# Kernel optimization log

Hardware: AMD Instinct MI355X
Metric: run time of the kernel (lower is better)

## Reference

```python
import jax, jax.numpy as jnp
import numpy as np

WS = 8      # window_size
SS = 4      # shift_size
DIM = 64
B, H, W = 4, 256, 256
EPS = 1e-12


def _conv(x, w, groups=1, pad=0):
    return jax.lax.conv_general_dilated(
        x, w, window_strides=(1, 1), padding=[(pad, pad), (pad, pad)],
        feature_group_count=groups,
        dimension_numbers=('NCHW', 'OIHW', 'NCHW'))


def _window_partition(x, ws):
    # Faithful to torch: permute (B,C,nh,ws,nw,ws)->(B,C,nh,nw,ws,ws) then flat view(-1,C,ws,ws)
    b, c, h, w = x.shape
    pb, pr = (-h) % ws, (-w) % ws
    if pb or pr:
        x = jnp.pad(x, ((0, 0), (0, 0), (0, pb), (0, pr)))
    h2, w2 = h + pb, w + pr
    x = x.reshape(b, c, h2 // ws, ws, w2 // ws, ws).transpose(0, 1, 2, 4, 3, 5)
    return x.reshape(-1, c, ws, ws)


def _window_reverse(win, ws, h, w):
    pb, pr = (-h) % ws, (-w) % ws
    h2, w2 = h + pb, w + pr
    b = win.shape[0] * ws * ws // (h2 * w2)
    x = win.reshape(b, -1, h2 // ws, w2 // ws, ws, ws).transpose(0, 1, 2, 4, 3, 5)
    x = x.reshape(b, -1, h2, w2)
    return x[:, :, :h, :w]


def _chan_attn(q, k, v, temp):
    # channel (transposed) attention on flattened window pixels
    n, c = q.shape[0], q.shape[1]
    q = q.reshape(n, c, -1)
    k = k.reshape(n, c, -1)
    v = v.reshape(n, c, -1)
    q = q / jnp.maximum(jnp.linalg.norm(q, axis=-1, keepdims=True), EPS)
    k = k / jnp.maximum(jnp.linalg.norm(k, axis=-1, keepdims=True), EPS)
    attn = jax.nn.softmax(jnp.einsum('ncd,nkd->nck', q, k) / temp, axis=-1)
    out = jnp.einsum('nck,nkd->ncd', attn, v)
    return out.reshape(n, c, WS, WS)


def setup_inputs() -> dict:
    key = jax.random.key(0)
    ks = jax.random.split(key, 10)
    C = DIM
    p = lambda k, s: jax.random.normal(k, s, jnp.float32) * 0.05
    return {
        'x': jax.random.normal(ks[0], (B, C, H, W), jnp.float32),
        'x_f': jax.random.normal(ks[1], (B, C, H, W), jnp.float32),
        'temperature': jnp.ones((1,), jnp.float32),
        'qk_w': p(ks[2], (2 * C, C, 1, 1)),
        'qk_dw_w': p(ks[3], (2 * C, 1, 3, 3)),
        'v_w': p(ks[4], (C, C, 1, 1)),
        'v_dw_w': p(ks[5], (C, 1, 3, 3)),
        'proj_w': p(ks[6], (C, C, 3, 3)),
        'proj1_w': p(ks[7], (C, C, 3, 3)),
        'qkv1_w': p(ks[8], (3 * C, C, 1, 1)),
        'qkv1_dw_w': p(ks[9], (3 * C, 1, 3, 3)),
    }


def reference(x, x_f, temperature, qk_w, qk_dw_w, v_w, v_dw_w,
              proj_w, proj1_w, qkv1_w, qkv1_dw_w):
    b, c, h, w = x.shape
    xw = _window_partition(x, WS)
    xfw = _window_partition(x_f, WS)

    qk = _conv(_conv(xfw, qk_w), qk_dw_w, groups=2 * c, pad=1)
    v = _conv(_conv(xw, v_w), v_dw_w, groups=c, pad=1)
    q, k = jnp.split(qk, 2, axis=1)
    out = _chan_attn(q, k, v, temperature)
    out = _conv(out, proj_w, pad=1)
    out = _window_reverse(out, WS, h, w)

    shift = jnp.roll(out, (-SS, -SS), axis=(2, 3))
    sw = _window_partition(shift, WS)
    qkv = _conv(_conv(sw, qkv1_w), qkv1_dw_w, groups=3 * c, pad=1)
    q, k, v = jnp.split(qkv, 3, axis=1)
    out = _chan_attn(q, k, v, temperature)
    out = _conv(out, proj1_w, pad=1)
    out = _window_reverse(out, WS, h, w)
    out = jnp.roll(out, (SS, SS), axis=(2, 3))
    return out
```

## Files before the change

### kernel.cpp

```cpp
#include <hip/hip_runtime.h>
#include <hip/hip_fp16.h>

typedef short v8s __attribute__((ext_vector_type(8)));
typedef float v4f __attribute__((ext_vector_type(4)));

#define MFMA_B16(a, b, c) __builtin_amdgcn_mfma_f32_16x16x32_bf16((a), (b), (c), 0, 0, 0)

#define XS 72
#define TS 68

__device__ __forceinline__ unsigned short bfr(float x) {
    unsigned u = __float_as_uint(x);
    u += 0x7fffu + ((u >> 16) & 1u);
    return (unsigned short)(u >> 16);
}

__device__ __forceinline__ void mm_stage_g(const unsigned short* __restrict__ Ag,
                                           const unsigned short* __restrict__ XB,
                                           float* __restrict__ T,
                                           int wv, int L, int q)
{
    v4f C[4];
#pragma unroll
    for (int nt = 0; nt < 4; ++nt) C[nt] = (v4f){0.f, 0.f, 0.f, 0.f};
#pragma unroll
    for (int kt = 0; kt < 2; ++kt) {
        v8s a = *(const v8s*)(Ag + (16 * wv + L) * 64 + kt * 32 + q * 8);
#pragma unroll
        for (int nt = 0; nt < 4; ++nt) {
            v8s b = *(const v8s*)(XB + (nt * 16 + L) * XS + kt * 32 + q * 8);
            C[nt] = MFMA_B16(a, b, C[nt]);
        }
    }
    const int rowb = 16 * wv + q * 4;
#pragma unroll
    for (int r = 0; r < 4; ++r) {
#pragma unroll
        for (int nt = 0; nt < 4; ++nt)
            T[(rowb + r) * TS + nt * 16 + L] = C[nt][r];
    }
}

template <bool TR, bool NORM>
__device__ __forceinline__ void dw_stage(const float* __restrict__ T,
                                         const float* __restrict__ dwg,
                                         unsigned short* __restrict__ M,
                                         int wv, int lane)
{
    const int c  = 16 * wv + (lane >> 2);
    const int r0 = (lane & 3) << 1;
    float w[9];
#pragma unroll
    for (int k = 0; k < 9; ++k) w[k] = dwg[c * 9 + k];
    float in[4][10];
#pragma unroll
    for (int r = 0; r < 4; ++r) {
        const int rr = r0 - 1 + r;
        in[r][0] = 0.f; in[r][9] = 0.f;
        if ((unsigned)rr < 8u) {
            float4 a = *(const float4*)(T + c * TS + rr * 8);
            float4 b = *(const float4*)(T + c * TS + rr * 8 + 4);
            in[r][1] = a.x; in[r][2] = a.y; in[r][3] = a.z; in[r][4] = a.w;
            in[r][5] = b.x; in[r][6] = b.y; in[r][7] = b.z; in[r][8] = b.w;
        } else {
#pragma unroll
            for (int j = 1; j < 9; ++j) in[r][j] = 0.f;
        }
    }
    float o[2][8];
#pragma unroll
    for (int rr = 0; rr < 2; ++rr)
#pragma unroll
        for (int j = 0; j < 8; ++j) {
            float s;
            s = w[0] * in[rr][j];
            s = fmaf(w[1], in[rr][j + 1], s);
            s = fmaf(w[2], in[rr][j + 2], s);
            s = fmaf(w[3], in[rr + 1][j], s);
            s = fmaf(w[4], in[rr + 1][j + 1], s);
            s = fmaf(w[5], in[rr + 1][j + 2], s);
            s = fmaf(w[6], in[rr + 2][j], s);
            s = fmaf(w[7], in[rr + 2][j + 1], s);
            s = fmaf(w[8], in[rr + 2][j + 2], s);
            o[rr][j] = s;
        }
    if (NORM) {
        float ss = 0.f;
#pragma unroll
        for (int rr = 0; rr < 2; ++rr)
#pragma unroll
            for (int j = 0; j < 8; ++j) ss = fmaf(o[rr][j], o[rr][j], ss);
        ss += __shfl_xor(ss, 1);
        ss += __shfl_xor(ss, 2);
        const float sc = 1.0f / fmaxf(sqrtf(ss), 1e-12f);
#pragma unroll
        for (int rr = 0; rr < 2; ++rr)
#pragma unroll
            for (int j = 0; j < 8; ++j) o[rr][j] *= sc;
    }
    if (TR) {
#pragma unroll
        for (int rr = 0; rr < 2; ++rr)
#pragma unroll
            for (int j = 0; j < 8; ++j)
                M[((r0 + rr) * 8 + j) * XS + c] = bfr(o[rr][j]);
    } else {
#pragma unroll
        for (int rr = 0; rr < 2; ++rr) {
            v8s v;
#pragma unroll
            for (int j = 0; j < 8; ++j) v[j] = (short)bfr(o[rr][j]);
            *(v8s*)(M + c * XS + (r0 + rr) * 8) = v;
        }
    }
}

__device__ __forceinline__ void mm_lds(const unsigned short* __restrict__ Am,
                                       const unsigned short* __restrict__ Bm,
                                       int wv, int L, int q, v4f C[4])
{
#pragma unroll
    for (int nt = 0; nt < 4; ++nt) C[nt] = (v4f){0.f, 0.f, 0.f, 0.f};
#pragma unroll
    for (int kt = 0; kt < 2; ++kt) {
        v8s a = *(const v8s*)(Am + (16 * wv + L) * XS + kt * 32 + q * 8);
#pragma unroll
        for (int nt = 0; nt < 4; ++nt) {
            v8s b = *(const v8s*)(Bm + (nt * 16 + L) * XS + kt * 32 + q * 8);
            C[nt] = MFMA_B16(a, b, C[nt]);
        }
    }
}

__device__ __forceinline__ void proj_mm(const unsigned short* __restrict__ Wg,
                                        const unsigned short* __restrict__ Ot,
                                        int wv, int L, int q, v4f C[4])
{
#pragma unroll
    for (int nt = 0; nt < 4; ++nt) C[nt] = (v4f){0.f, 0.f, 0.f, 0.f};
    const unsigned short* arow = Wg + (16 * wv + L) * 576;
    const int pc  = L & 7;
    const int prb = L >> 3;
#pragma unroll
    for (int tap = 0; tap < 9; ++tap) {
        const int dy = tap / 3 - 1, dx = tap % 3 - 1;
        const int spc = pc + dx;
        const bool vc = (unsigned)spc < 8u;
#pragma unroll
        for (int half = 0; half < 2; ++half) {
            v8s a = *(const v8s*)(arow + tap * 64 + half * 32 + q * 8);
#pragma unroll
            for (int nt = 0; nt < 4; ++nt) {
                const int spr = nt * 2 + prb + dy;
                v8s b = {0, 0, 0, 0, 0, 0, 0, 0};
                if (vc && (unsigned)spr < 8u)
                    b = *(const v8s*)(Ot + (spr * 8 + spc) * XS + half * 32 + q * 8);
                C[nt] = MFMA_B16(a, b, C[nt]);
            }
        }
    }
}

__device__ __forceinline__ void softmax_to_lds(v4f S[4], float invt,
                                               unsigned short* __restrict__ Am,
                                               int rowb, int L)
{
#pragma unroll
    for (int nt = 0; nt < 4; ++nt) S[nt] *= invt;
#pragma unroll
    for (int r = 0; r < 4; ++r) {
        float mx = fmaxf(fmaxf(S[0][r], S[1][r]), fmaxf(S[2][r], S[3][r]));
        mx = fmaxf(mx, __shfl_xor(mx, 1));
        mx = fmaxf(mx, __shfl_xor(mx, 2));
        mx = fmaxf(mx, __shfl_xor(mx, 4));
        mx = fmaxf(mx, __shfl_xor(mx, 8));
        float e0 = __expf(S[0][r] - mx);
        float e1 = __expf(S[1][r] - mx);
        float e2 = __expf(S[2][r] - mx);
        float e3 = __expf(S[3][r] - mx);
        float sm = e0 + e1 + e2 + e3;
        sm += __shfl_xor(sm, 1);
        sm += __shfl_xor(sm, 2);
        sm += __shfl_xor(sm, 4);
        sm += __shfl_xor(sm, 8);
        const float ri = 1.0f / sm;
        Am[(rowb + r) * XS + L +  0] = bfr(e0 * ri);
        Am[(rowb + r) * XS + L + 16] = bfr(e1 * ri);
        Am[(rowb + r) * XS + L + 32] = bfr(e2 * ri);
        Am[(rowb + r) * XS + L + 48] = bfr(e3 * ri);
    }
}

__global__ void prep(const float* __restrict__ qk_w, const float* __restrict__ v_w,
                     const float* __restrict__ qkv_w, const float* __restrict__ pw0,
                     const float* __restrict__ pw1, unsigned short* __restrict__ Wb)
{
    int i = blockIdx.x * 256 + threadIdx.x;
    float v;
    if (i < 8192) v = qk_w[i];
    else if (i < 12288) v = v_w[i - 8192];
    else if (i < 24576) v = qkv_w[i - 12288];
    else {
        int j = i - 24576;
        const float* s = pw0;
        if (j >= 36864) { s = pw1; j -= 36864; }
        const int o = j / 576, kk = j % 576;
        const int tap = kk >> 6, c = kk & 63;
        v = s[o * 576 + c * 9 + tap];
    }
    Wb[i] = bfr(v);
}

__global__ __launch_bounds__(256, 3) void k1(
    const float* __restrict__ x, const float* __restrict__ xf,
    const float* __restrict__ temp_p,
    const float* __restrict__ qk_dw, const float* __restrict__ v_dw,
    const unsigned short* __restrict__ Wqk, const unsigned short* __restrict__ Wv,
    const unsigned short* __restrict__ Wp0,
    __half* __restrict__ midh)
{
    __shared__ unsigned short XB[64 * XS];
    __shared__ float T[64 * TS];
    __shared__ unsigned short M0[64 * XS], M1[64 * XS], M2[64 * XS];

    const int t = threadIdx.x, n = blockIdx.x;
    const int lane = t & 63, wv = t >> 6, L = lane & 15, q = lane >> 4;
    const int rowb = 16 * wv + q * 4;
    const size_t base = (size_t)n << 12;
    const float invt = 1.0f / temp_p[0];

    const int yp = t >> 4, xx0 = (t & 15) << 4;
    const int c2b = (yp >> 3) << 5, ir = (yp & 7) << 3;

    {
        const float* src = xf + base + yp * 256 + xx0;
#pragma unroll
        for (int k = 0; k < 4; ++k) {
            float4 a = *(const float4*)(src + 4 * k);
            const int xx = xx0 + 4 * k;
            const int c = c2b + (xx >> 3), pb = ir + (xx & 7);
            XB[(pb + 0) * XS + c] = bfr(a.x);
            XB[(pb + 1) * XS + c] = bfr(a.y);
            XB[(pb + 2) * XS + c] = bfr(a.z);
            XB[(pb + 3) * XS + c] = bfr(a.w);
        }
    }
    __syncthreads();
    mm_stage_g(Wqk, XB, T, wv, L, q);
    __syncthreads();
    dw_stage<false, true>(T, qk_dw, M0, wv, lane);
    __syncthreads();
    mm_stage_g(Wqk + 4096, XB, T, wv, L, q);
    __syncthreads();
    dw_stage<false, true>(T, qk_dw + 576, M1, wv, lane);
    __syncthreads();

    float4 rx[4];
    {
        const float* src = x + base + yp * 256 + xx0;
#pragma unroll
        for (int k = 0; k < 4; ++k) rx[k] = *(const float4*)(src + 4 * k);
    }
    v4f S[4];
    mm_lds(M0, M1, wv, L, q, S);
    softmax_to_lds(S, invt, M0, rowb, L);
    {
#pragma unroll
        for (int k = 0; k < 4; ++k) {
            const int xx = xx0 + 4 * k;
            const int c = c2b + (xx >> 3), pb = ir + (xx & 7);
            XB[(pb + 0) * XS + c] = bfr(rx[k].x);
            XB[(pb + 1) * XS + c] = bfr(rx[k].y);
            XB[(pb + 2) * XS + c] = bfr(rx[k].z);
            XB[(pb + 3) * XS + c] = bfr(rx[k].w);
        }
    }
    __syncthreads();
    mm_stage_g(Wv, XB, T, wv, L, q);
    __syncthreads();
    dw_stage<true, false>(T, v_dw, M2, wv, lane);
    __syncthreads();
    v4f O[4];
    mm_lds(M0, M2, wv, L, q, O);
#pragma unroll
    for (int nt = 0; nt < 4; ++nt)
#pragma unroll
        for (int r = 0; r < 4; ++r)
            M1[(L + 16 * nt) * XS + (rowb + r)] = bfr(O[nt][r]);
    __syncthreads();
    v4f C[4];
    proj_mm(Wp0, M1, wv, L, q, C);
#pragma unroll
    for (int nt = 0; nt < 4; ++nt)
#pragma unroll
        for (int r = 0; r < 4; ++r) {
            const int o = rowb + r, p = L + 16 * nt;
            const int yy = ((o >> 5) << 3) + (p >> 3);
            const int xp = ((o & 31) << 3) + (p & 7);
            midh[base + yy * 256 + xp] = __float2half(C[nt][r]);
        }
}

__global__ __launch_bounds__(256, 3) void k2(
    const __half* __restrict__ midh, const float* __restrict__ temp_p,
    const float* __restrict__ qkv_dw,
    const unsigned short* __restrict__ Wqkv, const unsigned short* __restrict__ Wp1,
    float* __restrict__ out)
{
    __shared__ unsigned short XB[64 * XS];
    __shared__ float T[64 * TS];
    __shared__ unsigned short M0[64 * XS], M1[64 * XS], M2[64 * XS];

    const int t = threadIdx.x, m = blockIdx.x;
    const int lane = t & 63, wv = t >> 6, L = lane & 15, q = lane >> 4;
    const int rowb = 16 * wv + q * 4;
    const int plane = m >> 4, mh2 = m & 15;
    const __half* img = midh + ((size_t)plane << 16);
    const float invt = 1.0f / temp_p[0];

    {
        const int yp = t >> 4, xx0 = (t & 15) << 4;
        const int row = (mh2 * 16 + 4 + yp) & 255;
        const int c2b = (yp >> 3) << 5, ir = (yp & 7) << 3;
#pragma unroll
        for (int k = 0; k < 4; ++k) {
            const int cc = (xx0 + 4 + 4 * k) & 255;
            const __half2* hp = (const __half2*)(img + row * 256 + cc);
            __half2 h0 = hp[0], h1 = hp[1];
            const int xx = xx0 + 4 * k;
            const int c = c2b + (xx >> 3), pb = ir + (xx & 7);
            XB[(pb + 0) * XS + c] = bfr(__half2float(h0.x));
            XB[(pb + 1) * XS + c] = bfr(__half2float(h0.y));
            XB[(pb + 2) * XS + c] = bfr(__half2float(h1.x));
            XB[(pb + 3) * XS + c] = bfr(__half2float(h1.y));
        }
    }
    __syncthreads();
    mm_stage_g(Wqkv, XB, T, wv, L, q);
    __syncthreads();
    dw_stage<false, true>(T, qkv_dw, M0, wv, lane);
    __syncthreads();
    mm_stage_g(Wqkv + 4096, XB, T, wv, L, q);
    __syncthreads();
    dw_stage<false, true>(T, qkv_dw + 576, M1, wv, lane);
    __syncthreads();
    mm_stage_g(Wqkv + 8192, XB, T, wv, L, q);
    __syncthreads();
    dw_stage<true, false>(T, qkv_dw + 1152, M2, wv, lane);
    __syncthreads();
    v4f S[4];
    mm_lds(M0, M1, wv, L, q, S);
    softmax_to_lds(S, invt, M0, rowb, L);
    __syncthreads();
    v4f O[4];
    mm_lds(M0, M2, wv, L, q, O);
#pragma unroll
    for (int nt = 0; nt < 4; ++nt)
#pragma unroll
        for (int r = 0; r < 4; ++r)
            M1[(L + 16 * nt) * XS + (rowb + r)] = bfr(O[nt][r]);
    __syncthreads();
    v4f C[4];
    proj_mm(Wp1, M1, wv, L, q, C);
    float* op = out + ((size_t)plane << 16);
#pragma unroll
    for (int nt = 0; nt < 4; ++nt)
#pragma unroll
        for (int r = 0; r < 4; ++r) {
            const int o = rowb + r, p = L + 16 * nt;
            const int R = mh2 * 16 + ((o >> 5) << 3) + (p >> 3);
            const int orow = (R + 4) & 255;
            const int ocol = ((o & 31) * 8 + (p & 7) + 4) & 255;
            op[orow * 256 + ocol] = C[nt][r];
        }
}

extern "C" void kernel_launch(void* const* d_in, const int* in_sizes, int n_in,
                              void* d_out, int out_size, void* d_ws, size_t ws_size,
                              hipStream_t stream)
{
    const float* x       = (const float*)d_in[0];
    const float* xf      = (const float*)d_in[1];
    const float* temp    = (const float*)d_in[2];
    const float* qk_w    = (const float*)d_in[3];
    const float* qk_dw   = (const float*)d_in[4];
    const float* v_w     = (const float*)d_in[5];
    const float* v_dw    = (const float*)d_in[6];
    const float* proj_w  = (const float*)d_in[7];
    const float* proj1_w = (const float*)d_in[8];
    const float* qkv1_w  = (const float*)d_in[9];
    const float* qkv1_dw = (const float*)d_in[10];
    float* out = (float*)d_out;

    __half* midh = (__half*)d_ws;
    unsigned short* Wb = (unsigned short*)((char*)d_ws + 33554432);

    prep<<<384, 256, 0, stream>>>(qk_w, v_w, qkv1_w, proj_w, proj1_w, Wb);
    k1<<<4096, 256, 0, stream>>>(x, xf, temp, qk_dw, v_dw,
                                 Wb, Wb + 8192, Wb + 24576, midh);
    k2<<<4096, 256, 0, stream>>>(midh, temp, qkv1_dw,
                                 Wb + 12288, Wb + 61440, out);
}
```

Baseline: 350.1 us.

## Shrink shared memory with fp16 intermediates and batch 1x1 matmuls before depthwise stages

Replaces the fp32 T scratch buffer with fp16 values in four bf16-sized LDS buffers. This cuts shared memory per block so occupancy can rise from 3 to 4 blocks per CU, and launch bounds are raised to match. The 1x1 conv matmuls are now issued back to back, and the depthwise reads and writes are interleaved with fewer barriers. The intermediate image is now stored as bf16, so k2 loads it directly without conversion. The trade-off is lower precision for the intermediate and the pre-depthwise activations.

```diff
diff --git a/kernel.cpp b/kernel.cpp
--- a/kernel.cpp
+++ b/kernel.cpp
@@ -1,24 +1,28 @@
 #include <hip/hip_runtime.h>
-#include <hip/hip_fp16.h>
 
 typedef short v8s __attribute__((ext_vector_type(8)));
 typedef float v4f __attribute__((ext_vector_type(4)));
+typedef unsigned short u16;
 
 #define MFMA_B16(a, b, c) __builtin_amdgcn_mfma_f32_16x16x32_bf16((a), (b), (c), 0, 0, 0)
-
 #define XS 72
-#define TS 68
-
-__device__ __forceinline__ unsigned short bfr(float x) {
+
+__device__ __forceinline__ u16 bfr(float x) {
     unsigned u = __float_as_uint(x);
     u += 0x7fffu + ((u >> 16) & 1u);
-    return (unsigned short)(u >> 16);
-}
-
-__device__ __forceinline__ void mm_stage_g(const unsigned short* __restrict__ Ag,
-                                           const unsigned short* __restrict__ XB,
-                                           float* __restrict__ T,
-                                           int wv, int L, int q)
+    return (u16)(u >> 16);
+}
+__device__ __forceinline__ u16 f16r(float x) {
+    _Float16 h = (_Float16)x; u16 u; __builtin_memcpy(&u, &h, 2); return u;
+}
+__device__ __forceinline__ float f16f(u16 u) {
+    _Float16 h; __builtin_memcpy(&h, &u, 2); return (float)h;
+}
+
+__device__ __forceinline__ void mm_stage(const u16* __restrict__ Ag,
+                                         const u16* __restrict__ XB,
+                                         u16* __restrict__ M,
+                                         int wv, int L, int q)
 {
     v4f C[4];
 #pragma unroll
@@ -32,40 +36,39 @@
             C[nt] = MFMA_B16(a, b, C[nt]);
         }
     }
-    const int rowb = 16 * wv + q * 4;
+    const int rowb = 16 * wv + 4 * q;
+#pragma unroll
+    for (int r = 0; r < 4; ++r)
+#pragma unroll
+        for (int nt = 0; nt < 4; ++nt)
+            M[(rowb + r) * XS + nt * 16 + L] = f16r(C[nt][r]);
+}
+
+__device__ __forceinline__ void dw_read(const u16* __restrict__ M, int c, int r0,
+                                        v8s raw[4])
+{
 #pragma unroll
     for (int r = 0; r < 4; ++r) {
-#pragma unroll
-        for (int nt = 0; nt < 4; ++nt)
-            T[(rowb + r) * TS + nt * 16 + L] = C[nt][r];
+        const int rr = r0 - 1 + r;
+        raw[r] = ((unsigned)rr < 8u) ? *(const v8s*)(M + c * XS + rr * 8)
+                                     : (v8s){0, 0, 0, 0, 0, 0, 0, 0};
     }
 }
 
 template <bool TR, bool NORM>
-__device__ __forceinline__ void dw_stage(const float* __restrict__ T,
-                                         const float* __restrict__ dwg,
-                                         unsigned short* __restrict__ M,
-                                         int wv, int lane)
-{
-    const int c  = 16 * wv + (lane >> 2);
-    const int r0 = (lane & 3) << 1;
+__device__ __forceinline__ void dw_write(const float* __restrict__ dwg,
+                                         const v8s raw[4], int c, int r0,
+                                         u16* __restrict__ Out)
+{
     float w[9];
 #pragma unroll
     for (int k = 0; k < 9; ++k) w[k] = dwg[c * 9 + k];
     float in[4][10];
 #pragma unroll
     for (int r = 0; r < 4; ++r) {
-        const int rr = r0 - 1 + r;
         in[r][0] = 0.f; in[r][9] = 0.f;
-        if ((unsigned)rr < 8u) {
-            float4 a = *(const float4*)(T + c * TS + rr * 8);
-            float4 b = *(const float4*)(T + c * TS + rr * 8 + 4);
-            in[r][1] = a.x; in[r][2] = a.y; in[r][3] = a.z; in[r][4] = a.w;
-            in[r][5] = b.x; in[r][6] = b.y; in[r][7] = b.z; in[r][8] = b.w;
-        } else {
-#pragma unroll
-            for (int j = 1; j < 9; ++j) in[r][j] = 0.f;
-        }
+#pragma unroll
+        for (int j = 0; j < 8; ++j) in[r][j + 1] = f16f((u16)raw[r][j]);
     }
     float o[2][8];
 #pragma unroll
@@ -103,20 +106,20 @@
         for (int rr = 0; rr < 2; ++rr)
 #pragma unroll
             for (int j = 0; j < 8; ++j)
-                M[((r0 + rr) * 8 + j) * XS + c] = bfr(o[rr][j]);
+                Out[((r0 + rr) * 8 + j) * XS + c] = bfr(o[rr][j]);
     } else {
 #pragma unroll
         for (int rr = 0; rr < 2; ++rr) {
             v8s v;
 #pragma unroll
             for (int j = 0; j < 8; ++j) v[j] = (short)bfr(o[rr][j]);
-            *(v8s*)(M + c * XS + (r0 + rr) * 8) = v;
-        }
-    }
-}
-
-__device__ __forceinline__ void mm_lds(const unsigned short* __restrict__ Am,
-                                       const unsigned short* __restrict__ Bm,
+            *(v8s*)(Out + c * XS + (r0 + rr) * 8) = v;
+        }
+    }
+}
+
+__device__ __forceinline__ void mm_lds(const u16* __restrict__ Am,
+                                       const u16* __restrict__ Bm,
                                        int wv, int L, int q, v4f C[4])
 {
 #pragma unroll
@@ -132,14 +135,14 @@
     }
 }
 
-__device__ __forceinline__ void proj_mm(const unsigned short* __restrict__ Wg,
-                                        const unsigned short* __restrict__ Ot,
+__device__ __forceinline__ void proj_mm(const u16* __restrict__ Wg,
+                                        const u16* __restrict__ Ot,
                                         int wv, int L, int q, v4f C[4])
 {
 #pragma unroll
     for (int nt = 0; nt < 4; ++nt) C[nt] = (v4f){0.f, 0.f, 0.f, 0.f};
-    const unsigned short* arow = Wg + (16 * wv + L) * 576;
-    const int pc  = L & 7;
+    const u16* arow = Wg + (16 * wv + L) * 576;
+    const int pc = L & 7;
     const int prb = L >> 3;
 #pragma unroll
     for (int tap = 0; tap < 9; ++tap) {
@@ -162,7 +165,7 @@
 }
 
 __device__ __forceinline__ void softmax_to_lds(v4f S[4], float invt,
-                                               unsigned short* __restrict__ Am,
+                                               u16* __restrict__ Am,
                                                int rowb, int L)
 {
 #pragma unroll
@@ -193,7 +196,7 @@
 
 __global__ void prep(const float* __restrict__ qk_w, const float* __restrict__ v_w,
                      const float* __restrict__ qkv_w, const float* __restrict__ pw0,
-                     const float* __restrict__ pw1, unsigned short* __restrict__ Wb)
+                     const float* __restrict__ pw1, u16* __restrict__ Wb)
 {
     int i = blockIdx.x * 256 + threadIdx.x;
     float v;
@@ -211,85 +214,81 @@
     Wb[i] = bfr(v);
 }
 
-__global__ __launch_bounds__(256, 3) void k1(
+__global__ __launch_bounds__(256, 4) void k1(
     const float* __restrict__ x, const float* __restrict__ xf,
     const float* __restrict__ temp_p,
     const float* __restrict__ qk_dw, const float* __restrict__ v_dw,
-    const unsigned short* __restrict__ Wqk, const unsigned short* __restrict__ Wv,
-    const unsigned short* __restrict__ Wp0,
-    __half* __restrict__ midh)
-{
-    __shared__ unsigned short XB[64 * XS];
-    __shared__ float T[64 * TS];
-    __shared__ unsigned short M0[64 * XS], M1[64 * XS], M2[64 * XS];
-
+    const u16* __restrict__ Wqk, const u16* __restrict__ Wv,
+    const u16* __restrict__ Wp0,
+    u16* __restrict__ midb)
+{
+    __shared__ u16 B0[64 * XS], B1[64 * XS], B2[64 * XS], B3[64 * XS];
     const int t = threadIdx.x, n = blockIdx.x;
     const int lane = t & 63, wv = t >> 6, L = lane & 15, q = lane >> 4;
-    const int rowb = 16 * wv + q * 4;
+    const int rowb = 16 * wv + 4 * q;
     const size_t base = (size_t)n << 12;
     const float invt = 1.0f / temp_p[0];
-
     const int yp = t >> 4, xx0 = (t & 15) << 4;
     const int c2b = (yp >> 3) << 5, ir = (yp & 7) << 3;
-
+    const int dc = t >> 2, dr0 = (t & 3) << 1;
+
+    float4 rx[4];
     {
-        const float* src = xf + base + yp * 256 + xx0;
+        const float* sf = xf + base + yp * 256 + xx0;
+        const float* sx = x  + base + yp * 256 + xx0;
 #pragma unroll
         for (int k = 0; k < 4; ++k) {
-            float4 a = *(const float4*)(src + 4 * k);
+            float4 a = *(const float4*)(sf + 4 * k);
+            rx[k] = *(const float4*)(sx + 4 * k);
             const int xx = xx0 + 4 * k;
             const int c = c2b + (xx >> 3), pb = ir + (xx & 7);
-            XB[(pb + 0) * XS + c] = bfr(a.x);
-            XB[(pb + 1) * XS + c] = bfr(a.y);
-            XB[(pb + 2) * XS + c] = bfr(a.z);
-            XB[(pb + 3) * XS + c] = bfr(a.w);
-        }
-    }
-    __syncthreads();
-    mm_stage_g(Wqk, XB, T, wv, L, q);
-    __syncthreads();
-    dw_stage<false, true>(T, qk_dw, M0, wv, lane);
-    __syncthreads();
-    mm_stage_g(Wqk + 4096, XB, T, wv, L, q);
-    __syncthreads();
-    dw_stage<false, true>(T, qk_dw + 576, M1, wv, lane);
-    __syncthreads();
-
-    float4 rx[4];
-    {
-        const float* src = x + base + yp * 256 + xx0;
-#pragma unroll
-        for (int k = 0; k < 4; ++k) rx[k] = *(const float4*)(src + 4 * k);
-    }
-    v4f S[4];
-    mm_lds(M0, M1, wv, L, q, S);
-    softmax_to_lds(S, invt, M0, rowb, L);
+            B0[(pb + 0) * XS + c] = bfr(a.x);
+            B0[(pb + 1) * XS + c] = bfr(a.y);
+            B0[(pb + 2) * XS + c] = bfr(a.z);
+            B0[(pb + 3) * XS + c] = bfr(a.w);
+        }
+    }
+    __syncthreads();
+    mm_stage(Wqk,        B0, B1, wv, L, q);
+    mm_stage(Wqk + 4096, B0, B2, wv, L, q);
+    __syncthreads();
     {
 #pragma unroll
         for (int k = 0; k < 4; ++k) {
             const int xx = xx0 + 4 * k;
             const int c = c2b + (xx >> 3), pb = ir + (xx & 7);
-            XB[(pb + 0) * XS + c] = bfr(rx[k].x);
-            XB[(pb + 1) * XS + c] = bfr(rx[k].y);
-            XB[(pb + 2) * XS + c] = bfr(rx[k].z);
-            XB[(pb + 3) * XS + c] = bfr(rx[k].w);
-        }
-    }
-    __syncthreads();
-    mm_stage_g(Wv, XB, T, wv, L, q);
-    __syncthreads();
-    dw_stage<true, false>(T, v_dw, M2, wv, lane);
+            B3[(pb + 0) * XS + c] = bfr(rx[k].x);
+            B3[(pb + 1) * XS + c] = bfr(rx[k].y);
+            B3[(pb + 2) * XS + c] = bfr(rx[k].z);
+            B3[(pb + 3) * XS + c] = bfr(rx[k].w);
+        }
+    }
+    v8s rawA[4];
+    dw_read(B1, dc, dr0, rawA);
+    __syncthreads();
+    mm_stage(Wv, B3, B0, wv, L, q);
+    dw_write<false, true>(qk_dw, rawA, dc, dr0, B1);
+    v8s rawB[4];
+    dw_read(B2, dc, dr0, rawB);
+    __syncthreads();
+    dw_write<false, true>(qk_dw + 576, rawB, dc, dr0, B2);
+    dw_read(B0, dc, dr0, rawA);
+    dw_write<true, false>(v_dw, rawA, dc, dr0, B3);
+    __syncthreads();
+    v4f S[4];
+    mm_lds(B1, B2, wv, L, q, S);
+    softmax_to_lds(S, invt, B1, rowb, L);
     __syncthreads();
     v4f O[4];
-    mm_lds(M0, M2, wv, L, q, O);
+    mm_lds(B1, B3, wv, L, q, O);
 #pragma unroll
     for (int nt = 0; nt < 4; ++nt)
 #pragma unroll
         for (int r = 0; r < 4; ++r)
-            M1[(L + 16 * nt) * XS + (rowb + r)] = bfr(O[nt][r]);
+            B2[(L + 16 * nt) * XS + rowb + r] = bfr(O[nt][r]);
     __syncthreads();
     v4f C[4];
-    proj_mm(Wp0, M1, wv, L, q, C);
+    proj_mm(Wp0, B2, wv, L, q, C);
 #pragma unroll
     for (int nt = 0; nt < 4; ++nt)
 #pragma unroll
@@ -297,71 +296,72 @@
             const int o = rowb + r, p = L + 16 * nt;
             const int yy = ((o >> 5) << 3) + (p >> 3);
             const int xp = ((o & 31) << 3) + (p & 7);
-            midh[base + yy * 256 + xp] = __float2half(C[nt][r]);
-        }
-}
-
-__global__ __launch_bounds__(256, 3) void k2(
-    const __half* __restrict__ midh, const float* __restrict__ temp_p,
+            midb[base + yy * 256 + xp] = bfr(C[nt][r]);
+        }
+}
+
+__global__ __launch_bounds__(256, 4) void k2(
+    const u16* __restrict__ midb, const float* __restrict__ temp_p,
     const float* __restrict__ qkv_dw,
-    const unsigned short* __restrict__ Wqkv, const unsigned short* __restrict__ Wp1,
+    const u16* __restrict__ Wqkv, const u16* __restrict__ Wp1,
     float* __restrict__ out)
 {
-    __shared__ unsigned short XB[64 * XS];
-    __shared__ float T[64 * TS];
-    __shared__ unsigned short M0[64 * XS], M1[64 * XS], M2[64 * XS];
-
+    __shared__ u16 B0[64 * XS], B1[64 * XS], B2[64 * XS], B3[64 * XS];
     const int t = threadIdx.x, m = blockIdx.x;
     const int lane = t & 63, wv = t >> 6, L = lane & 15, q = lane >> 4;
-    const int rowb = 16 * wv + q * 4;
+    const int rowb = 16 * wv + 4 * q;
     const int plane = m >> 4, mh2 = m & 15;
-    const __half* img = midh + ((size_t)plane << 16);
+    const u16* img = midb + ((size_t)plane << 16);
     const float invt = 1.0f / temp_p[0];
+    const int yp = t >> 4, xx0 = (t & 15) << 4;
+    const int c2b = (yp >> 3) << 5, ir = (yp & 7) << 3;
+    const int dc = t >> 2, dr0 = (t & 3) << 1;
 
     {
-        const int yp = t >> 4, xx0 = (t & 15) << 4;
         const int row = (mh2 * 16 + 4 + yp) & 255;
-        const int c2b = (yp >> 3) << 5, ir = (yp & 7) << 3;
 #pragma unroll
         for (int k = 0; k < 4; ++k) {
             const int cc = (xx0 + 4 + 4 * k) & 255;
-            const __half2* hp = (const __half2*)(img + row * 256 + cc);
-            __half2 h0 = hp[0], h1 = hp[1];
+            ushort4 a = *(const ushort4*)(img + row * 256 + cc);
             const int xx = xx0 + 4 * k;
             const int c = c2b + (xx >> 3), pb = ir + (xx & 7);
-            XB[(pb + 0) * XS + c] = bfr(__half2float(h0.x));
-            XB[(pb + 1) * XS + c] = bfr(__half2float(h0.y));
-            XB[(pb + 2) * XS + c] = bfr(__half2float(h1.x));
-            XB[(pb + 3) * XS + c] = bfr(__half2float(h1.y));
-        }
-    }
-    __syncthreads();
-    mm_stage_g(Wqkv, XB, T, wv, L, q);
-    __syncthreads();
-    dw_stage<false, true>(T, qkv_dw, M0, wv, lane);
-    __syncthreads();
-    mm_stage_g(Wqkv + 4096, XB, T, wv, L, q);
-    __syncthreads();
-    dw_stage<false, true>(T, qkv_dw + 576, M1, wv, lane);
-    __syncthreads();
-    mm_stage_g(Wqkv + 8192, XB, T, wv, L, q);
-    __syncthreads();
-    dw_stage<true, false>(T, qkv_dw + 1152, M2, wv, lane);
+            B0[(pb + 0) * XS + c] = a.x;
+            B0[(pb + 1) * XS + c] = a.y;
+            B0[(pb + 2) * XS + c] = a.z;
+            B0[(pb + 3) * XS + c] = a.w;
+        }
+    }
+    __syncthreads();
+    mm_stage(Wqkv,        B0, B1, wv, L, q);
+    mm_stage(Wqkv + 4096, B0, B2, wv, L, q);
+    mm_stage(Wqkv + 8192, B0, B3, wv, L, q);
+    __syncthreads();
+    v8s rawV[4];
+    dw_read(B3, dc, dr0, rawV);
+    dw_write<true, false>(qkv_dw + 1152, rawV, dc, dr0, B0);
+    v8s rawQ[4];
+    dw_read(B1, dc, dr0, rawQ);
+    __syncthreads();
+    dw_write<false, true>(qkv_dw, rawQ, dc, dr0, B1);
+    v8s rawK[4];
+    dw_read(B2, dc, dr0, rawK);
+    __syncthreads();
+    dw_write<false, true>(qkv_dw + 576, rawK, dc, dr0, B2);
     __syncthreads();
     v4f S[4];
-    mm_lds(M0, M1, wv, L, q, S);
-    softmax_to_lds(S, invt, M0, rowb, L);
+    mm_lds(B1, B2, wv, L, q, S);
+    softmax_to_lds(S, invt, B1, rowb, L);
     __syncthreads();
     v4f O[4];
-    mm_lds(M0, M2, wv, L, q, O);
+    mm_lds(B1, B0, wv, L, q, O);
 #pragma unroll
     for (int nt = 0; nt < 4; ++nt)
 #pragma unroll
         for (int r = 0; r < 4; ++r)
-            M1[(L + 16 * nt) * XS + (rowb + r)] = bfr(O[nt][r]);
+            B3[(L + 16 * nt) * XS + rowb + r] = bfr(O[nt][r]);
     __syncthreads();
     v4f C[4];
-    proj_mm(Wp1, M1, wv, L, q, C);
+    proj_mm(Wp1, B3, wv, L, q, C);
     float* op = out + ((size_t)plane << 16);
 #pragma unroll
     for (int nt = 0; nt < 4; ++nt)
@@ -392,12 +392,12 @@
     const float* qkv1_dw = (const float*)d_in[10];
     float* out = (float*)d_out;
 
-    __half* midh = (__half*)d_ws;
-    unsigned short* Wb = (unsigned short*)((char*)d_ws + 33554432);
+    u16* midb = (u16*)d_ws;
+    u16* Wb   = (u16*)((char*)d_ws + 33554432);
 
     prep<<<384, 256, 0, stream>>>(qk_w, v_w, qkv1_w, proj_w, proj1_w, Wb);
     k1<<<4096, 256, 0, stream>>>(x, xf, temp, qk_dw, v_dw,
-                                 Wb, Wb + 8192, Wb + 24576, midh);
-    k2<<<4096, 256, 0, stream>>>(midh, temp, qkv1_dw,
+                                 Wb, Wb + 8192, Wb + 24576, midb);
+    k2<<<4096, 256, 0, stream>>>(midb, temp, qkv1_dw,
                                  Wb + 12288, Wb + 61440, out);
 }
```

Result: faster. 292.5 us (-16.5%).
